# Kernel tuning notes

Hardware: AMD Instinct MI355X
Metric: run time of the kernel (lower is better)

Reference implementation:

```python
import jax, jax.numpy as jnp
import numpy as np

NUM_QUERIES = 900
EMBED_DIM = 256
NUM_HEADS = 8
EPS = 1e-5


def bilinear_sample(feats, grid):
    """F.grid_sample(..., align_corners=False, padding_mode='zeros', bilinear).
    feats: [BN, C, H, W], grid: [BN, Q, 2] in [-1,1] (x, y). Returns [BN, Q, C]."""
    BN, C, H, W = feats.shape
    ix = (grid[..., 0] + 1.0) * (W * 0.5) - 0.5
    iy = (grid[..., 1] + 1.0) * (H * 0.5) - 0.5
    x0 = jnp.floor(ix)
    y0 = jnp.floor(iy)
    wx1 = ix - x0
    wy1 = iy - y0
    x0i = x0.astype(jnp.int32)
    y0i = y0.astype(jnp.int32)
    x1i = x0i + 1
    y1i = y0i + 1
    b = jnp.arange(BN)[:, None]

    def gather(yy, xx):
        inb = (xx >= 0) & (xx < W) & (yy >= 0) & (yy < H)
        yc = jnp.clip(yy, 0, H - 1)
        xc = jnp.clip(xx, 0, W - 1)
        v = feats[b, :, yc, xc]  # [BN, Q, C]
        return v * inb[..., None].astype(feats.dtype)

    out = (gather(y0i, x0i) * ((1 - wx1) * (1 - wy1))[..., None]
           + gather(y0i, x1i) * (wx1 * (1 - wy1))[..., None]
           + gather(y1i, x0i) * ((1 - wx1) * wy1)[..., None]
           + gather(y1i, x1i) * (wx1 * wy1)[..., None])
    return out


def setup_inputs() -> dict:
    key = jax.random.key(0)
    ks = jax.random.split(key, 16)
    B, N, C, H, W = 2, 6, 256, 116, 200
    Q, D = NUM_QUERIES, EMBED_DIM
    s = 0.02
    return {
        "image_features": jax.random.normal(ks[0], (B, N, C, H, W), jnp.float32),
        "lidar2img": jax.random.normal(ks[1], (B, N, 4, 4), jnp.float32),
        "query_embedding": jax.random.normal(ks[2], (Q, D), jnp.float32) * s,
        "ref_w": jax.random.normal(ks[3], (3, D), jnp.float32) * s,
        "ref_b": jnp.zeros((3,), jnp.float32),
        "in_proj_w": jax.random.normal(ks[4], (3 * D, D), jnp.float32) * s,
        "in_proj_b": jnp.zeros((3 * D,), jnp.float32),
        "out_proj_w": jax.random.normal(ks[5], (D, D), jnp.float32) * s,
        "out_proj_b": jnp.zeros((D,), jnp.float32),
        "norm_w": jnp.ones((D,), jnp.float32),
        "norm_b": jnp.zeros((D,), jnp.float32),
        "cls_w": jax.random.normal(ks[6], (2, D), jnp.float32) * s,
        "cls_b": jnp.zeros((2,), jnp.float32),
        "box_w": jax.random.normal(ks[7], (6, D), jnp.float32) * s,
        "box_b": jnp.zeros((6,), jnp.float32),
    }


def reference(image_features, lidar2img, query_embedding, ref_w, ref_b,
              in_proj_w, in_proj_b, out_proj_w, out_proj_b,
              norm_w, norm_b, cls_w, cls_b, box_w, box_b):
    B, N, C, H, W = image_features.shape
    Q, D = query_embedding.shape

    q = jnp.broadcast_to(query_embedding[None], (B, Q, D))

    # reference points in [0,1]^3
    ref = jax.nn.sigmoid(q @ ref_w.T + ref_b)  # [B,Q,3]

    # 3D -> 2D projection per camera
    homo = jnp.concatenate([ref, jnp.ones_like(ref[..., :1])], axis=-1)  # [B,Q,4]
    p2h = jnp.einsum('bnij,bqj->bnqi', lidar2img, homo)  # [B,N,Q,4]
    z = p2h[..., 2:3]
    pts2d = p2h[..., 0:2] / (jnp.abs(z) + 1e-5)  # [B,N,Q,2]
    mask = (z > 1e-5)[..., 0]  # [B,N,Q]

    # normalize to [-1,1]
    pn = jnp.stack([pts2d[..., 0] / (W - 1) * 2 - 1,
                    pts2d[..., 1] / (H - 1) * 2 - 1], axis=-1)  # [B,N,Q,2]

    feats_flat = image_features.reshape(B * N, C, H, W)
    grid = pn.reshape(B * N, Q, 2)
    sampled = bilinear_sample(feats_flat, grid)            # [BN,Q,C]
    sampled = sampled.reshape(B, N, Q, C).transpose(0, 2, 1, 3)  # [B,Q,N,C]

    mask_t = mask.transpose(0, 2, 1)[..., None]  # [B,Q,N,1]
    # faithful to torch .view(B,Q,N,2): a raw row-major reshape, not a transpose
    pn_view = pn.reshape(B, Q, N, 2)
    valid = mask_t & (jnp.max(jnp.abs(pn_view), axis=-1, keepdims=True) < 1)  # [B,Q,N,1]
    validf = valid.astype(sampled.dtype)

    sum_feats = jnp.sum(sampled * validf, axis=2)  # [B,Q,C]
    count = jnp.clip(jnp.sum(validf, axis=2), 1.0, None)
    tgt = sum_feats / count

    x = q + tgt  # [B,Q,D]

    # MultiheadAttention (batch_first, 8 heads, no dropout)
    qkv = x @ in_proj_w.T + in_proj_b
    qh, kh, vh = jnp.split(qkv, 3, axis=-1)
    hd = D // NUM_HEADS
    def heads(t):
        return t.reshape(B, Q, NUM_HEADS, hd).transpose(0, 2, 1, 3)  # [B,h,Q,hd]
    qh, kh, vh = heads(qh), heads(kh), heads(vh)
    scores = jnp.einsum('bhqd,bhkd->bhqk', qh, kh) / jnp.sqrt(jnp.asarray(hd, x.dtype))
    attn = jax.nn.softmax(scores, axis=-1)
    o = jnp.einsum('bhqk,bhkd->bhqd', attn, vh).transpose(0, 2, 1, 3).reshape(B, Q, D)
    o = o @ out_proj_w.T + out_proj_b

    # LayerNorm (no residual, faithful to the module)
    mu = jnp.mean(o, axis=-1, keepdims=True)
    var = jnp.mean((o - mu) ** 2, axis=-1, keepdims=True)
    xn = (o - mu) / jnp.sqrt(var + EPS) * norm_w + norm_b

    box = xn @ box_w.T + box_b
    box = jnp.concatenate([jax.nn.sigmoid(box[..., :3]), box[..., 3:]], axis=-1)
    cls = xn @ cls_w.T + cls_b
    return cls, box
```

## Files before the change

### kernel.cpp

```cpp
#include <hip/hip_runtime.h>
#include <math.h>

#define BB 2
#define NCAM 6
#define CC 256
#define HH 116
#define WW 200
#define QQ 900
#define DD 256
#define NHD 8
#define HD 32
#define HWSZ (HH*WW)

__device__ __forceinline__ float sigmoidf_(float x){ return 1.0f/(1.0f+expf(-x)); }

__global__ void ref_kernel(const float* __restrict__ qe, const float* __restrict__ ref_w,
                           const float* __restrict__ ref_b, float* __restrict__ ref) {
    int idx = blockIdx.x*256 + threadIdx.x;
    if (idx >= QQ*3) return;
    int q = idx/3, j = idx%3;
    float acc = ref_b[j];
    const float* qr = qe + q*DD;
    const float* wr = ref_w + j*DD;
    for (int k=0;k<DD;k++) acc += qr[k]*wr[k];
    ref[idx] = sigmoidf_(acc);
}

__global__ void proj_kernel(const float* __restrict__ l2i, const float* __restrict__ ref,
        float* __restrict__ wxa, float* __restrict__ wya,
        int* __restrict__ x0a, int* __restrict__ y0a,
        int* __restrict__ maskz, int* __restrict__ inimg) {
    int idx = blockIdx.x*256+threadIdx.x;
    if (idx >= BB*NCAM*QQ) return;
    int q = idx % QQ;
    int bn = idx / QQ;
    float h0 = ref[q*3+0], h1 = ref[q*3+1], h2 = ref[q*3+2];
    const float* m = l2i + bn*16;
    float px = m[0]*h0+m[1]*h1+m[2]*h2+m[3];
    float py = m[4]*h0+m[5]*h1+m[6]*h2+m[7];
    float pz = m[8]*h0+m[9]*h1+m[10]*h2+m[11];
    float denom = fabsf(pz)+1e-5f;
    float sx = px/denom, sy = py/denom;
    float pnx = sx/(float)(WW-1)*2.0f-1.0f;
    float pny = sy/(float)(HH-1)*2.0f-1.0f;
    maskz[idx] = (pz > 1e-5f) ? 1 : 0;
    inimg[idx] = (fmaxf(fabsf(pnx),fabsf(pny)) < 1.0f) ? 1 : 0;
    float ix = (pnx+1.0f)*(WW*0.5f)-0.5f;
    float iy = (pny+1.0f)*(HH*0.5f)-0.5f;
    float x0f = floorf(ix), y0f = floorf(iy);
    wxa[idx] = ix-x0f; wya[idx] = iy-y0f;
    x0a[idx] = (int)x0f; y0a[idx] = (int)y0f;
}

__global__ __launch_bounds__(256) void sample_kernel(const float* __restrict__ feats,
        const float* __restrict__ qe, const float* __restrict__ wxa, const float* __restrict__ wya,
        const int* __restrict__ x0a, const int* __restrict__ y0a,
        const int* __restrict__ maskz, const int* __restrict__ inimg,
        float* __restrict__ xout) {
    int bq = blockIdx.x;
    int b = bq / QQ, q = bq % QQ;
    int c = threadIdx.x;
    float sum = 0.0f;
    int cnt = 0;
    for (int n = 0; n < NCAM; n++) {
        int s = (b*NCAM+n)*QQ + q;
        int sq = b*(NCAM*QQ) + q*NCAM + n;
        int v = maskz[s] & inimg[sq];
        if (!v) continue;
        cnt++;
        float wx = wxa[s], wy = wya[s];
        int x0 = x0a[s], y0 = y0a[s];
        int x1 = x0+1, y1 = y0+1;
        const float* fb = feats + ((size_t)(b*NCAM+n)*CC + c)*HWSZ;
        float w00 = (1.f-wx)*(1.f-wy), w10 = wx*(1.f-wy), w01 = (1.f-wx)*wy, w11 = wx*wy;
        bool xin0 = ((unsigned)x0 < (unsigned)WW);
        bool xin1 = ((unsigned)x1 < (unsigned)WW);
        if ((unsigned)y0 < (unsigned)HH) {
            const float* row = fb + y0*WW;
            if (xin0) sum += w00*row[x0];
            if (xin1) sum += w10*row[x1];
        }
        if ((unsigned)y1 < (unsigned)HH) {
            const float* row = fb + y1*WW;
            if (xin0) sum += w01*row[x0];
            if (xin1) sum += w11*row[x1];
        }
    }
    float tgt = sum / (float)(cnt > 0 ? cnt : 1);
    xout[(size_t)bq*DD + c] = qe[q*DD+c] + tgt;
}

#define TILE 64
#define BKK 16
__global__ __launch_bounds__(256) void sgemm_nt(const float* __restrict__ A,
        const float* __restrict__ Bw, const float* __restrict__ bias,
        float* __restrict__ Cm, int M, int N, int K) {
    __shared__ float As[BKK][TILE];
    __shared__ float Bs[BKK][TILE];
    int tid = threadIdx.x;
    int m0 = blockIdx.y * TILE, n0 = blockIdx.x * TILE;
    float acc[4][4] = {};
    int tx = tid & 15, ty = tid >> 4;
    for (int k0 = 0; k0 < K; k0 += BKK) {
        #pragma unroll
        for (int i = 0; i < 4; i++) {
            int idx = tid + i * 256;
            int m = idx >> 4;
            int k = idx & 15;
            int gm = m0 + m;
            As[k][m] = (gm < M) ? A[(size_t)gm * K + k0 + k] : 0.0f;
            int gn = n0 + m;
            Bs[k][m] = (gn < N) ? Bw[(size_t)gn * K + k0 + k] : 0.0f;
        }
        __syncthreads();
        #pragma unroll
        for (int k = 0; k < BKK; k++) {
            float a[4], bb[4];
            #pragma unroll
            for (int i = 0; i < 4; i++) a[i] = As[k][ty*4+i];
            #pragma unroll
            for (int j = 0; j < 4; j++) bb[j] = Bs[k][tx*4+j];
            #pragma unroll
            for (int i = 0; i < 4; i++)
                #pragma unroll
                for (int j = 0; j < 4; j++)
                    acc[i][j] += a[i] * bb[j];
        }
        __syncthreads();
    }
    for (int i = 0; i < 4; i++) {
        int gm = m0 + ty*4 + i;
        if (gm >= M) continue;
        for (int j = 0; j < 4; j++) {
            int gn = n0 + tx*4 + j;
            if (gn < N) Cm[(size_t)gm * N + gn] = acc[i][j] + bias[gn];
        }
    }
}

#define QTILE 32
#define KTILE 64
#define NQB 29
__global__ __launch_bounds__(256) void attn_flash(const float* __restrict__ qkv,
                                                  float* __restrict__ attn_out) {
    __shared__ __align__(16) float Qs[32][36];
    __shared__ __align__(16) float Ks[32][68];
    __shared__ __align__(16) float Vs[64][36];
    __shared__ __align__(16) float Ps[32][68];
    int blk = blockIdx.x;
    int qb = blk % NQB;
    int h  = (blk / NQB) % NHD;
    int b  = blk / (NQB*NHD);
    int q0 = qb * QTILE;
    int tid = threadIdx.x;
    int tx = tid & 15, ty = tid >> 4;

    {
        int q = tid >> 3;
        int dseg = (tid & 7) * 4;
        int gq = q0 + q; if (gq > QQ-1) gq = QQ-1;
        const float4 f = *(const float4*)(qkv + ((size_t)(b*QQ+gq))*768 + h*HD + dseg);
        Qs[dseg+0][q] = f.x; Qs[dseg+1][q] = f.y; Qs[dseg+2][q] = f.z; Qs[dseg+3][q] = f.w;
    }

    float O[2][2] = {};
    float l[2] = {0.f, 0.f};
    const float scale = 0.17677669529663689f;

    for (int k0 = 0; k0 < QQ; k0 += KTILE) {
        {
            int k = tid >> 2;
            int dseg = (tid & 3) * 8;
            int gk = k0 + k; if (gk > QQ-1) gk = QQ-1;
            const float* kp = qkv + ((size_t)(b*QQ+gk))*768 + 256 + h*HD + dseg;
            float4 f0 = *(const float4*)(kp);
            float4 f1 = *(const float4*)(kp+4);
            Ks[dseg+0][k]=f0.x; Ks[dseg+1][k]=f0.y; Ks[dseg+2][k]=f0.z; Ks[dseg+3][k]=f0.w;
            Ks[dseg+4][k]=f1.x; Ks[dseg+5][k]=f1.y; Ks[dseg+6][k]=f1.z; Ks[dseg+7][k]=f1.w;
            const float* vp = qkv + ((size_t)(b*QQ+gk))*768 + 512 + h*HD + dseg;
            *(float4*)(&Vs[k][dseg])   = *(const float4*)(vp);
            *(float4*)(&Vs[k][dseg+4]) = *(const float4*)(vp+4);
        }
        __syncthreads();

        float acc[2][4] = {};
        #pragma unroll
        for (int d = 0; d < 32; d++) {
            float a0 = Qs[d][ty*2];
            float a1 = Qs[d][ty*2+1];
            float4 bk = *(const float4*)(&Ks[d][tx*4]);
            acc[0][0] += a0*bk.x; acc[0][1] += a0*bk.y; acc[0][2] += a0*bk.z; acc[0][3] += a0*bk.w;
            acc[1][0] += a1*bk.x; acc[1][1] += a1*bk.y; acc[1][2] += a1*bk.z; acc[1][3] += a1*bk.w;
        }
        #pragma unroll
        for (int i = 0; i < 2; i++) {
            float e[4];
            float rs = 0.f;
            #pragma unroll
            for (int j = 0; j < 4; j++) {
                int gk = k0 + tx*4 + j;
                float v = (gk < QQ) ? expf(acc[i][j]*scale) : 0.f;
                e[j] = v; rs += v;
            }
            #pragma unroll
            for (int m = 1; m < 16; m <<= 1) rs += __shfl_xor(rs, m, 16);
            l[i] += rs;
            *(float4*)(&Ps[ty*2+i][tx*4]) = make_float4(e[0],e[1],e[2],e[3]);
        }
        __syncthreads();

        #pragma unroll
        for (int k4 = 0; k4 < 16; k4++) {
            float4 p0 = *(const float4*)(&Ps[ty*2][k4*4]);
            float4 p1 = *(const float4*)(&Ps[ty*2+1][k4*4]);
            float2 v0 = *(const float2*)(&Vs[k4*4+0][tx*2]);
            float2 v1 = *(const float2*)(&Vs[k4*4+1][tx*2]);
            float2 v2 = *(const float2*)(&Vs[k4*4+2][tx*2]);
            float2 v3 = *(const float2*)(&Vs[k4*4+3][tx*2]);
            O[0][0] += p0.x*v0.x + p0.y*v1.x + p0.z*v2.x + p0.w*v3.x;
            O[0][1] += p0.x*v0.y + p0.y*v1.y + p0.z*v2.y + p0.w*v3.y;
            O[1][0] += p1.x*v0.x + p1.y*v1.x + p1.z*v2.x + p1.w*v3.x;
            O[1][1] += p1.x*v0.y + p1.y*v1.y + p1.z*v2.y + p1.w*v3.y;
        }
        __syncthreads();
    }

    #pragma unroll
    for (int i = 0; i < 2; i++) {
        int gq = q0 + ty*2 + i;
        if (gq < QQ) {
            float inv = 1.0f / l[i];
            float* op = attn_out + ((size_t)(b*QQ+gq))*DD + h*HD + tx*2;
            op[0] = O[i][0]*inv;
            op[1] = O[i][1]*inv;
        }
    }
}

__global__ __launch_bounds__(256) void final_kernel(const float* __restrict__ o,
    const float* __restrict__ norm_w, const float* __restrict__ norm_b,
    const float* __restrict__ cls_w, const float* __restrict__ cls_b,
    const float* __restrict__ box_w, const float* __restrict__ box_b,
    float* __restrict__ out) {
    __shared__ float s_xn[DD];
    __shared__ float red[8];
    int bq = blockIdx.x;
    int t = threadIdx.x;
    float val = o[(size_t)bq*DD + t];
    float v1 = val, v2 = val*val;
    for (int off=32; off>0; off>>=1) { v1 += __shfl_down(v1, off); v2 += __shfl_down(v2, off); }
    if ((t & 63) == 0) { red[t>>6] = v1; red[4 + (t>>6)] = v2; }
    __syncthreads();
    float ssum = red[0]+red[1]+red[2]+red[3];
    float ssq  = red[4]+red[5]+red[6]+red[7];
    float mu = ssum / (float)DD;
    float var = ssq / (float)DD - mu*mu;
    float inv = 1.0f / sqrtf(var + 1e-5f);
    s_xn[t] = (val - mu)*inv*norm_w[t] + norm_b[t];
    __syncthreads();
    int j = t >> 5, lane = t & 31;
    const float* wrow = (j < 2) ? (cls_w + j*DD) : (box_w + (j-2)*DD);
    float acc = 0.f;
    for (int k=lane; k<DD; k+=32) acc += s_xn[k]*wrow[k];
    for (int off=16; off>0; off>>=1) acc += __shfl_down(acc, off, 32);
    if (lane == 0) {
        if (j < 2) {
            out[(size_t)bq*2 + j] = acc + cls_b[j];
        } else {
            int jj = j-2;
            float v = acc + box_b[jj];
            if (jj < 3) v = sigmoidf_(v);
            out[BB*QQ*2 + (size_t)bq*6 + jj] = v;
        }
    }
}

extern "C" void kernel_launch(void* const* d_in, const int* in_sizes, int n_in,
                              void* d_out, int out_size, void* d_ws, size_t ws_size,
                              hipStream_t stream) {
    const float* feats = (const float*)d_in[0];
    const float* l2i   = (const float*)d_in[1];
    const float* qe    = (const float*)d_in[2];
    const float* ref_w = (const float*)d_in[3];
    const float* ref_b = (const float*)d_in[4];
    const float* ipw   = (const float*)d_in[5];
    const float* ipb   = (const float*)d_in[6];
    const float* opw   = (const float*)d_in[7];
    const float* opb   = (const float*)d_in[8];
    const float* nw    = (const float*)d_in[9];
    const float* nb    = (const float*)d_in[10];
    const float* clsw  = (const float*)d_in[11];
    const float* clsb  = (const float*)d_in[12];
    const float* boxw  = (const float*)d_in[13];
    const float* boxb  = (const float*)d_in[14];
    float* out = (float*)d_out;
    float* ws = (float*)d_ws;

    float* ref   = ws;
    float* wxa   = ws + 2700;
    float* wya   = wxa + 10800;
    int*   x0a   = (int*)(wya + 10800);
    int*   y0a   = x0a + 10800;
    int*   maskz = y0a + 10800;
    int*   inimg = maskz + 10800;
    float* x     = (float*)(inimg + 10800);
    float* qkv   = x + 460800;
    float* attn  = qkv + 1382400;
    float* oproj = attn + 460800;

    ref_kernel<<<(QQ*3+255)/256, 256, 0, stream>>>(qe, ref_w, ref_b, ref);
    proj_kernel<<<(BB*NCAM*QQ+255)/256, 256, 0, stream>>>(l2i, ref, wxa, wya, x0a, y0a, maskz, inimg);
    sample_kernel<<<BB*QQ, 256, 0, stream>>>(feats, qe, wxa, wya, x0a, y0a, maskz, inimg, x);
    sgemm_nt<<<dim3(768/TILE, (BB*QQ+TILE-1)/TILE), 256, 0, stream>>>(x, ipw, ipb, qkv, BB*QQ, 768, 256);
    attn_flash<<<BB*NHD*NQB, 256, 0, stream>>>(qkv, attn);
    sgemm_nt<<<dim3(256/TILE, (BB*QQ+TILE-1)/TILE), 256, 0, stream>>>(attn, opw, opb, oproj, BB*QQ, 256, 256);
    final_kernel<<<BB*QQ, 256, 0, stream>>>(oproj, nw, nb, clsw, clsb, boxw, boxb, out);
}
```

Before: 504.4 us.

## Batch sampling gathers via shared weights and enlarge attention query tile

The sampling kernel now has six threads precompute per-camera bilinear weights and offsets into shared memory. Every channel thread then issues all 24 gathers up front so the loads can be in flight together, replacing a serial loop with dependent branches. The attention kernel doubles its query tile to 64 with a 4x4 register block per thread, which halves the number of times K/V are reloaded and raises arithmetic intensity. In exchange the attention kernel uses more registers and launches fewer blocks (240 instead of 464), which may leave the GPU underfilled.

Measured after the change: 507.7 us. No clear change (+0.6%).

```diff
diff --git a/kernel.cpp b/kernel.cpp
--- a/kernel.cpp
+++ b/kernel.cpp
@@ -57,37 +57,61 @@
         const int* __restrict__ x0a, const int* __restrict__ y0a,
         const int* __restrict__ maskz, const int* __restrict__ inimg,
         float* __restrict__ xout) {
+    __shared__ float smw[NCAM][4];
+    __shared__ int   smo[NCAM][4];
+    __shared__ float sv[NCAM];
     int bq = blockIdx.x;
     int b = bq / QQ, q = bq % QQ;
     int c = threadIdx.x;
-    float sum = 0.0f;
-    int cnt = 0;
-    for (int n = 0; n < NCAM; n++) {
-        int s = (b*NCAM+n)*QQ + q;
+    float qv = qe[q*DD + c];
+    if (threadIdx.x < NCAM) {
+        int n = threadIdx.x;
+        int s  = (b*NCAM+n)*QQ + q;
         int sq = b*(NCAM*QQ) + q*NCAM + n;
         int v = maskz[s] & inimg[sq];
-        if (!v) continue;
-        cnt++;
         float wx = wxa[s], wy = wya[s];
         int x0 = x0a[s], y0 = y0a[s];
         int x1 = x0+1, y1 = y0+1;
+        bool x0ok = ((unsigned)x0 < (unsigned)WW);
+        bool x1ok = ((unsigned)x1 < (unsigned)WW);
+        bool y0ok = ((unsigned)y0 < (unsigned)HH);
+        bool y1ok = ((unsigned)y1 < (unsigned)HH);
+        int cx0 = x0ok ? x0 : 0, cx1 = x1ok ? x1 : 0;
+        int cy0 = y0ok ? y0 : 0, cy1 = y1ok ? y1 : 0;
+        float fv = v ? 1.f : 0.f;
+        smw[n][0] = (y0ok && x0ok) ? fv*(1.f-wx)*(1.f-wy) : 0.f;
+        smw[n][1] = (y0ok && x1ok) ? fv*wx*(1.f-wy)       : 0.f;
+        smw[n][2] = (y1ok && x0ok) ? fv*(1.f-wx)*wy       : 0.f;
+        smw[n][3] = (y1ok && x1ok) ? fv*wx*wy             : 0.f;
+        smo[n][0] = cy0*WW + cx0;
+        smo[n][1] = cy0*WW + cx1;
+        smo[n][2] = cy1*WW + cx0;
+        smo[n][3] = cy1*WW + cx1;
+        sv[n] = fv;
+    }
+    __syncthreads();
+    float wreg[NCAM][4];
+    float vreg[NCAM][4];
+    #pragma unroll
+    for (int n = 0; n < NCAM; n++) {
         const float* fb = feats + ((size_t)(b*NCAM+n)*CC + c)*HWSZ;
-        float w00 = (1.f-wx)*(1.f-wy), w10 = wx*(1.f-wy), w01 = (1.f-wx)*wy, w11 = wx*wy;
-        bool xin0 = ((unsigned)x0 < (unsigned)WW);
-        bool xin1 = ((unsigned)x1 < (unsigned)WW);
-        if ((unsigned)y0 < (unsigned)HH) {
-            const float* row = fb + y0*WW;
-            if (xin0) sum += w00*row[x0];
-            if (xin1) sum += w10*row[x1];
-        }
-        if ((unsigned)y1 < (unsigned)HH) {
-            const float* row = fb + y1*WW;
-            if (xin0) sum += w01*row[x0];
-            if (xin1) sum += w11*row[x1];
-        }
-    }
-    float tgt = sum / (float)(cnt > 0 ? cnt : 1);
-    xout[(size_t)bq*DD + c] = qe[q*DD+c] + tgt;
+        #pragma unroll
+        for (int k = 0; k < 4; k++) {
+            float w = smw[n][k];
+            wreg[n][k] = w;
+            vreg[n][k] = 0.f;
+            if (w != 0.f) vreg[n][k] = fb[smo[n][k]];
+        }
+    }
+    float sum = 0.f;
+    #pragma unroll
+    for (int n = 0; n < NCAM; n++)
+        #pragma unroll
+        for (int k = 0; k < 4; k++)
+            sum += wreg[n][k]*vreg[n][k];
+    float cf = sv[0]+sv[1]+sv[2]+sv[3]+sv[4]+sv[5];
+    float inv = 1.0f / fmaxf(cf, 1.0f);
+    xout[(size_t)bq*DD + c] = qv + sum*inv;
 }
 
 #define TILE 64
@@ -138,36 +162,39 @@
     }
 }
 
-#define QTILE 32
-#define KTILE 64
-#define NQB 29
-__global__ __launch_bounds__(256) void attn_flash(const float* __restrict__ qkv,
-                                                  float* __restrict__ attn_out) {
-    __shared__ __align__(16) float Qs[32][36];
-    __shared__ __align__(16) float Ks[32][68];
+#define QT2 64
+#define KT2 64
+#define NQB2 15
+__global__ __launch_bounds__(256) void attn_flash2(const float* __restrict__ qkv,
+                                                   float* __restrict__ attn_out) {
+    __shared__ __align__(16) float Qs[32][72];
+    __shared__ __align__(16) float Ks[32][72];
     __shared__ __align__(16) float Vs[64][36];
-    __shared__ __align__(16) float Ps[32][68];
+    __shared__ __align__(16) float Ps[64][76];
     int blk = blockIdx.x;
-    int qb = blk % NQB;
-    int h  = (blk / NQB) % NHD;
-    int b  = blk / (NQB*NHD);
-    int q0 = qb * QTILE;
+    int qb = blk % NQB2;
+    int h  = (blk / NQB2) % NHD;
+    int b  = blk / (NQB2*NHD);
+    int q0 = qb * QT2;
     int tid = threadIdx.x;
     int tx = tid & 15, ty = tid >> 4;
 
     {
-        int q = tid >> 3;
-        int dseg = (tid & 7) * 4;
+        int q = tid >> 2;
+        int dseg = (tid & 3) * 8;
         int gq = q0 + q; if (gq > QQ-1) gq = QQ-1;
-        const float4 f = *(const float4*)(qkv + ((size_t)(b*QQ+gq))*768 + h*HD + dseg);
-        Qs[dseg+0][q] = f.x; Qs[dseg+1][q] = f.y; Qs[dseg+2][q] = f.z; Qs[dseg+3][q] = f.w;
-    }
-
-    float O[2][2] = {};
-    float l[2] = {0.f, 0.f};
+        const float* qp = qkv + ((size_t)(b*QQ+gq))*768 + h*HD + dseg;
+        float4 f0 = *(const float4*)(qp);
+        float4 f1 = *(const float4*)(qp+4);
+        Qs[dseg+0][q]=f0.x; Qs[dseg+1][q]=f0.y; Qs[dseg+2][q]=f0.z; Qs[dseg+3][q]=f0.w;
+        Qs[dseg+4][q]=f1.x; Qs[dseg+5][q]=f1.y; Qs[dseg+6][q]=f1.z; Qs[dseg+7][q]=f1.w;
+    }
+
+    float O[4][2] = {};
+    float l[4] = {};
     const float scale = 0.17677669529663689f;
 
-    for (int k0 = 0; k0 < QQ; k0 += KTILE) {
+    for (int k0 = 0; k0 < QQ; k0 += KT2) {
         {
             int k = tid >> 2;
             int dseg = (tid & 3) * 8;
@@ -183,17 +210,18 @@
         }
         __syncthreads();
 
-        float acc[2][4] = {};
+        float acc[4][4] = {};
         #pragma unroll
         for (int d = 0; d < 32; d++) {
-            float a0 = Qs[d][ty*2];
-            float a1 = Qs[d][ty*2+1];
-            float4 bk = *(const float4*)(&Ks[d][tx*4]);
-            acc[0][0] += a0*bk.x; acc[0][1] += a0*bk.y; acc[0][2] += a0*bk.z; acc[0][3] += a0*bk.w;
-            acc[1][0] += a1*bk.x; acc[1][1] += a1*bk.y; acc[1][2] += a1*bk.z; acc[1][3] += a1*bk.w;
-        }
-        #pragma unroll
-        for (int i = 0; i < 2; i++) {
+            float4 qv = *(const float4*)(&Qs[d][ty*4]);
+            float4 kv = *(const float4*)(&Ks[d][tx*4]);
+            acc[0][0]+=qv.x*kv.x; acc[0][1]+=qv.x*kv.y; acc[0][2]+=qv.x*kv.z; acc[0][3]+=qv.x*kv.w;
+            acc[1][0]+=qv.y*kv.x; acc[1][1]+=qv.y*kv.y; acc[1][2]+=qv.y*kv.z; acc[1][3]+=qv.y*kv.w;
+            acc[2][0]+=qv.z*kv.x; acc[2][1]+=qv.z*kv.y; acc[2][2]+=qv.z*kv.z; acc[2][3]+=qv.z*kv.w;
+            acc[3][0]+=qv.w*kv.x; acc[3][1]+=qv.w*kv.y; acc[3][2]+=qv.w*kv.z; acc[3][3]+=qv.w*kv.w;
+        }
+        #pragma unroll
+        for (int i = 0; i < 4; i++) {
             float e[4];
             float rs = 0.f;
             #pragma unroll
@@ -205,34 +233,34 @@
             #pragma unroll
             for (int m = 1; m < 16; m <<= 1) rs += __shfl_xor(rs, m, 16);
             l[i] += rs;
-            *(float4*)(&Ps[ty*2+i][tx*4]) = make_float4(e[0],e[1],e[2],e[3]);
+            *(float4*)(&Ps[ty*4+i][tx*4]) = make_float4(e[0],e[1],e[2],e[3]);
         }
         __syncthreads();
 
         #pragma unroll
         for (int k4 = 0; k4 < 16; k4++) {
-            float4 p0 = *(const float4*)(&Ps[ty*2][k4*4]);
-            float4 p1 = *(const float4*)(&Ps[ty*2+1][k4*4]);
-            float2 v0 = *(const float2*)(&Vs[k4*4+0][tx*2]);
-            float2 v1 = *(const float2*)(&Vs[k4*4+1][tx*2]);
-            float2 v2 = *(const float2*)(&Vs[k4*4+2][tx*2]);
-            float2 v3 = *(const float2*)(&Vs[k4*4+3][tx*2]);
-            O[0][0] += p0.x*v0.x + p0.y*v1.x + p0.z*v2.x + p0.w*v3.x;
-            O[0][1] += p0.x*v0.y + p0.y*v1.y + p0.z*v2.y + p0.w*v3.y;
-            O[1][0] += p1.x*v0.x + p1.y*v1.x + p1.z*v2.x + p1.w*v3.x;
-            O[1][1] += p1.x*v0.y + p1.y*v1.y + p1.z*v2.y + p1.w*v3.y;
+            float4 p[4];
+            float2 v[4];
+            #pragma unroll
+            for (int i = 0; i < 4; i++) p[i] = *(const float4*)(&Ps[ty*4+i][k4*4]);
+            #pragma unroll
+            for (int r = 0; r < 4; r++) v[r] = *(const float2*)(&Vs[k4*4+r][tx*2]);
+            #pragma unroll
+            for (int i = 0; i < 4; i++) {
+                O[i][0] += p[i].x*v[0].x + p[i].y*v[1].x + p[i].z*v[2].x + p[i].w*v[3].x;
+                O[i][1] += p[i].x*v[0].y + p[i].y*v[1].y + p[i].z*v[2].y + p[i].w*v[3].y;
+            }
         }
         __syncthreads();
     }
 
     #pragma unroll
-    for (int i = 0; i < 2; i++) {
-        int gq = q0 + ty*2 + i;
+    for (int i = 0; i < 4; i++) {
+        int gq = q0 + ty*4 + i;
         if (gq < QQ) {
             float inv = 1.0f / l[i];
-            float* op = attn_out + ((size_t)(b*QQ+gq))*DD + h*HD + tx*2;
-            op[0] = O[i][0]*inv;
-            op[1] = O[i][1]*inv;
+            float2 o2 = make_float2(O[i][0]*inv, O[i][1]*inv);
+            *(float2*)(attn_out + ((size_t)(b*QQ+gq))*DD + h*HD + tx*2) = o2;
         }
     }
 }
@@ -312,7 +340,7 @@
     proj_kernel<<<(BB*NCAM*QQ+255)/256, 256, 0, stream>>>(l2i, ref, wxa, wya, x0a, y0a, maskz, inimg);
     sample_kernel<<<BB*QQ, 256, 0, stream>>>(feats, qe, wxa, wya, x0a, y0a, maskz, inimg, x);
     sgemm_nt<<<dim3(768/TILE, (BB*QQ+TILE-1)/TILE), 256, 0, stream>>>(x, ipw, ipb, qkv, BB*QQ, 768, 256);
-    attn_flash<<<BB*NHD*NQB, 256, 0, stream>>>(qkv, attn);
+    attn_flash2<<<BB*NHD*NQB2, 256, 0, stream>>>(qkv, attn);
     sgemm_nt<<<dim3(256/TILE, (BB*QQ+TILE-1)/TILE), 256, 0, stream>>>(attn, opw, opb, oproj, BB*QQ, 256, 256);
     final_kernel<<<BB*QQ, 256, 0, stream>>>(oproj, nw, nb, clsw, clsb, boxw, boxb, out);
 }
```
